# Optimization experiments

Measured on AMD Instinct MI355X. Metric: run time of the kernel, lower is better.

The kernel has to match this reference:

```python
import jax, jax.numpy as jnp
import numpy as np

DIM = 1024
DFF = 4096
B, L = 4, 4096


def _lin_init(key, din, dout):
    k1, k2 = jax.random.split(key)
    bound = 1.0 / np.sqrt(din)
    w = jax.random.uniform(k1, (din, dout), jnp.float32, -bound, bound)
    b = jax.random.uniform(k2, (dout,), jnp.float32, -bound, bound)
    return w, b


def setup_inputs() -> dict:
    key = jax.random.key(0)
    ks = jax.random.split(key, 12)
    x = jax.random.normal(ks[0], (B, L, DIM), jnp.float32)
    hidden = jax.random.normal(ks[1], (B, DIM), jnp.float32)
    w_ln_z, b_ln_z = _lin_init(ks[2], DIM, DIM)
    w_dt, b_dt = _lin_init(ks[3], DIM, DIM)
    w_y, b_y = _lin_init(ks[4], DIM, DIM)
    w_yg, b_yg = _lin_init(ks[5], DIM, DIM)
    w_ff, b_ff = _lin_init(ks[6], DIM, DFF)
    w_ffg, b_ffg = _lin_init(ks[7], DIM, DFF)
    w_ffo, b_ffo = _lin_init(ks[8], DFF, DIM)
    g_sio = jnp.ones((DIM,), jnp.float32)
    g_ffn = jnp.ones((DIM,), jnp.float32)
    return dict(x=x, hidden=hidden, w_ln_z=w_ln_z, b_ln_z=b_ln_z, w_dt=w_dt,
                b_dt=b_dt, w_y=w_y, b_y=b_y, w_yg=w_yg, b_yg=b_yg,
                w_ff=w_ff, b_ff=b_ff, w_ffg=w_ffg, b_ffg=b_ffg,
                w_ffo=w_ffo, b_ffo=b_ffo, g_sio=g_sio, g_ffn=g_ffn)


def _rmsnorm(x, g, eps=1e-6):
    return x * jax.lax.rsqrt(jnp.mean(x * x, axis=-1, keepdims=True) + eps) * g


def reference(x, hidden, w_ln_z, b_ln_z, w_dt, b_dt, w_y, b_y, w_yg, b_yg,
              w_ff, b_ff, w_ffg, b_ffg, w_ffo, b_ffo, g_sio, g_ffn):
    silu = jax.nn.silu
    sp = jax.nn.softplus
    # --- SioConv branch ---
    residual = x
    xn = _rmsnorm(x, g_sio)
    dt = xn @ w_dt + b_dt
    ln_z = -sp(-(xn @ w_ln_z + b_ln_z))
    ln_da = -sp(-dt)           # log sigmoid(dt)
    ln_o_da = -sp(dt)          # log sigmoid(-dt)
    ln_o_da_cumsum = jnp.cumsum(ln_o_da, axis=1)
    lcse = jax.lax.cumlogsumexp(ln_z + ln_da - ln_o_da_cumsum, axis=1)
    h_inner = jnp.exp(lcse + ln_o_da_cumsum)                 # [B,L,D]
    h_cross = jnp.exp(ln_o_da_cumsum) * hidden[:, None, :]   # [B,L,D]
    h = h_inner + h_cross
    y = (h @ w_y + b_y) * silu(xn @ w_yg + b_yg)
    x = y + residual
    # --- FFN branch ---
    residual = x
    xn = _rmsnorm(x, g_ffn)
    ff = ((xn @ w_ff + b_ff) * silu(xn @ w_ffg + b_ffg)) @ w_ffo + b_ffo
    x = ff + residual
    return (x, h)
```

## Files before the change

kernel.cpp:

```cpp
#include <hip/hip_runtime.h>
#include <cstdint>
#include <cstddef>

using u16 = unsigned short;
using bf16x8 = __attribute__((ext_vector_type(8))) short;
using f32x4  = __attribute__((ext_vector_type(4))) float;

__device__ __forceinline__ u16 f2bf(float f) {
  unsigned u = __float_as_uint(f);
  u += 0x7fffu + ((u >> 16) & 1u);
  return (u16)(u >> 16);
}
__device__ __forceinline__ float bf2f(u16 h) {
  return __uint_as_float(((unsigned)h) << 16);
}

__device__ __forceinline__ void gload_lds16(const void* g, void* l) {
  auto gp = reinterpret_cast<const __attribute__((address_space(1))) char*>(
      reinterpret_cast<uintptr_t>(g));
  auto lp = reinterpret_cast<__attribute__((address_space(3))) char*>(
      reinterpret_cast<uintptr_t>(l));
  __builtin_amdgcn_global_load_lds(gp, lp, 16, 0, 0);
}

__global__ __launch_bounds__(256) void transpose_to_bf16(
    const float* __restrict__ W, u16* __restrict__ WT, int din, int dout) {
  __shared__ float tile[32][33];
  const int j0 = blockIdx.x * 32;
  const int i0 = blockIdx.y * 32;
  const int tx = threadIdx.x & 31;
  const int ty = threadIdx.x >> 5;
#pragma unroll
  for (int k = 0; k < 32; k += 8)
    tile[ty + k][tx] = W[(size_t)(i0 + ty + k) * dout + (j0 + tx)];
  __syncthreads();
#pragma unroll
  for (int k = 0; k < 32; k += 8)
    WT[(size_t)(j0 + ty + k) * din + (i0 + tx)] = f2bf(tile[tx][ty + k]);
}

__global__ __launch_bounds__(256) void rmsnorm_kernel(
    const float* __restrict__ x, const float* __restrict__ g, u16* __restrict__ xn) {
  const int row = blockIdx.x;
  const float4 v = ((const float4*)(x + (size_t)row * 1024))[threadIdx.x];
  float ss = v.x * v.x + v.y * v.y + v.z * v.z + v.w * v.w;
#pragma unroll
  for (int off = 32; off > 0; off >>= 1) ss += __shfl_down(ss, off, 64);
  __shared__ float red[4];
  if ((threadIdx.x & 63) == 0) red[threadIdx.x >> 6] = ss;
  __syncthreads();
  const float rs = rsqrtf((red[0] + red[1] + red[2] + red[3]) * (1.f / 1024.f) + 1e-6f);
  const float4 gv = ((const float4*)g)[threadIdx.x];
  ushort4 o;
  o.x = f2bf(v.x * rs * gv.x);
  o.y = f2bf(v.y * rs * gv.y);
  o.z = f2bf(v.z * rs * gv.z);
  o.w = f2bf(v.w * rs * gv.w);
  ((ushort4*)(xn + (size_t)row * 1024))[threadIdx.x] = o;
}

__global__ __launch_bounds__(256) void scan_pass1(
    const u16* __restrict__ dt, const u16* __restrict__ lnz,
    float* __restrict__ P, float* __restrict__ S) {
  const int blk = blockIdx.x;
  const int dblk = blk & 3;
  const int chunk = (blk >> 2) & 63;
  const int b = blk >> 8;
  const int d = dblk * 256 + threadIdx.x;
  const size_t base = ((size_t)b * 4096 + (size_t)chunk * 64) * 1024 + d;
  float p = 1.f, s = 0.f;
#pragma unroll 8
  for (int l = 0; l < 64; ++l) {
    const float dtv = bf2f(dt[base + (size_t)l * 1024]);
    const float zv = bf2f(lnz[base + (size_t)l * 1024]);
    const float a = 1.f / (1.f + __expf(dtv));
    const float zs = 1.f / (1.f + __expf(-zv));
    const float in = (1.f - a) * zs;
    p *= a;
    s = a * s + in;
  }
  const size_t o = ((size_t)b * 64 + chunk) * 1024 + d;
  P[o] = p;
  S[o] = s;
}

__global__ __launch_bounds__(256) void scan_pass2(
    const float* __restrict__ P, const float* __restrict__ S,
    const float* __restrict__ hidden, float* __restrict__ hin) {
  const int idx = blockIdx.x * 256 + threadIdx.x;
  const int b = idx >> 10, d = idx & 1023;
  float h = hidden[idx];
#pragma unroll 8
  for (int c = 0; c < 64; ++c) {
    const size_t o = ((size_t)b * 64 + c) * 1024 + d;
    hin[o] = h;
    h = P[o] * h + S[o];
  }
}

__global__ __launch_bounds__(256) void scan_pass3(
    const u16* __restrict__ dt, const u16* __restrict__ lnz,
    const float* __restrict__ hin, float* __restrict__ h_out, u16* __restrict__ hbf) {
  const int blk = blockIdx.x;
  const int dblk = blk & 3;
  const int chunk = (blk >> 2) & 63;
  const int b = blk >> 8;
  const int d = dblk * 256 + threadIdx.x;
  const size_t base = ((size_t)b * 4096 + (size_t)chunk * 64) * 1024 + d;
  float h = hin[((size_t)b * 64 + chunk) * 1024 + d];
#pragma unroll 4
  for (int l = 0; l < 64; ++l) {
    const float dtv = bf2f(dt[base + (size_t)l * 1024]);
    const float zv = bf2f(lnz[base + (size_t)l * 1024]);
    const float a = 1.f / (1.f + __expf(dtv));
    const float zs = 1.f / (1.f + __expf(-zv));
    h = a * h + (1.f - a) * zs;
    h_out[base + (size_t)l * 1024] = h;
    hbf[base + (size_t)l * 1024] = f2bf(h);
  }
}

template <int EPI>
__global__ __launch_bounds__(512, 4) void gemm256(
    const u16* __restrict__ A, const u16* __restrict__ B,
    const float* __restrict__ bias, const u16* __restrict__ gate,
    const float* __restrict__ resid, float* __restrict__ outF,
    u16* __restrict__ outH, u16* __restrict__ outH2, u16* __restrict__ outH3,
    int ntx, int N, int K) {
  constexpr int SLOT = 16384;
  const int tid = threadIdx.x;
  const int lane = tid & 63;
  const int wid = tid >> 6;
  const int wrow = wid >> 1;
  const int wcol = wid & 1;
  const int whalf = wrow >> 1;
  const int wsub  = wrow & 1;

  const int nwg = gridDim.x;
  int id = blockIdx.x;
  id = (id & 7) * (nwg >> 3) + (id >> 3);
  const int m0 = (id / ntx) * 256;
  const int n0 = (id % ntx) * 128;

  __shared__ __align__(16) char lds[5 * SLOT];

  f32x4 acc[4][4];
#pragma unroll
  for (int m = 0; m < 4; ++m)
#pragma unroll
    for (int n = 0; n < 4; ++n) acc[m][n] = (f32x4){0.f, 0.f, 0.f, 0.f};

  bf16x8 aR[2];
  bf16x8 bR[4][2];

  int aOff[4], bOff[4];
  {
    const int lq = (lane >> 4) << 4;
#pragma unroll
    for (int m = 0; m < 4; ++m) {
      const int hr = wsub * 64 + m * 16 + (lane & 15);
      aOff[m] = hr * 128 + (lq ^ ((hr & 7) << 4));
    }
#pragma unroll
    for (int n = 0; n < 4; ++n) {
      const int hr = wcol * 64 + n * 16 + (lane & 15);
      bOff[n] = hr * 128 + (lq ^ ((hr & 7) << 4));
    }
  }

  const int row0 = tid >> 3;
  const int kb0  = ((tid & 7) * 16) ^ ((row0 & 7) << 4);
  const size_t dRow = (size_t)128 * K;
  const char* pA0 = (const char*)A + (size_t)(m0 + row0) * K * 2 + kb0;
  const char* pA1 = pA0 + (size_t)256 * K;
  const char* pB  = (const char*)B + (size_t)(n0 + row0) * K * 2 + kb0;
  const int ldst = tid * 16;

#define STAGE(PTR, SB)                                                        \
  {                                                                           \
    gload_lds16(PTR, lds + (SB) + ldst);                                      \
    gload_lds16(PTR + dRow, lds + (SB) + ldst + 8192);                        \
    PTR += 128;                                                               \
  }

#define READA(SAB, Q)                                                         \
  {                                                                           \
    const int _o = aOff[Q];                                                   \
    aR[0] = *(const bf16x8*)(lds + (SAB) + _o);                               \
    aR[1] = *(const bf16x8*)(lds + (SAB) + (_o ^ 64));                        \
  }

#define READB(SBB)                                                            \
  _Pragma("unroll") for (int n = 0; n < 4; ++n) {                             \
    const int _o = bOff[n];                                                   \
    bR[n][0] = *(const bf16x8*)(lds + (SBB) + _o);                            \
    bR[n][1] = *(const bf16x8*)(lds + (SBB) + (_o ^ 64));                     \
  }

#define MMAQ(Q)                                                               \
  __builtin_amdgcn_s_setprio(1);                                              \
  _Pragma("unroll") for (int n = 0; n < 4; ++n)                               \
  _Pragma("unroll") for (int k = 0; k < 2; ++k)                               \
      acc[Q][n] = __builtin_amdgcn_mfma_f32_16x16x32_bf16(                    \
          aR[k], bR[n][k], acc[Q][n], 0, 0, 0);                               \
  __builtin_amdgcn_s_setprio(0);

  const int NT = K >> 6;

  STAGE(pB,  0 * SLOT);
  STAGE(pA0, 1 * SLOT);
  STAGE(pA1, 2 * SLOT);
  asm volatile("s_waitcnt vmcnt(0)" ::: "memory");
  __builtin_amdgcn_s_barrier();

  int iB = 0;

  for (int t = 0; t < NT; ++t) {
    int ib1 = iB + 1 + whalf; if (ib1 >= 5) ib1 -= 5;
    const int sAb = __builtin_amdgcn_readfirstlane(ib1 * SLOT);
    const int sBb = __builtin_amdgcn_readfirstlane(iB * SLOT);
    int i0s = iB + 3; if (i0s >= 5) i0s -= 5;
    int i1s = iB + 4; if (i1s >= 5) i1s -= 5;
    const int s0 = i0s * SLOT, s1 = i1s * SLOT, s2 = iB * SLOT;
    const bool st = (t < NT - 1);
    READB(sBb);
    READA(sAb, 0);
    if (st) STAGE(pB, s0);
    MMAQ(0);
    READA(sAb, 1);
    if (st) STAGE(pA0, s1);
    MMAQ(1);
    READA(sAb, 2);
    MMAQ(2);
    __builtin_amdgcn_s_barrier();
    READA(sAb, 3);
    if (st) STAGE(pA1, s2);
    MMAQ(3);
    asm volatile("s_waitcnt vmcnt(0)" ::: "memory");
    __builtin_amdgcn_s_barrier();
    iB += 3; if (iB >= 5) iB -= 5;
  }

#pragma unroll
  for (int m = 0; m < 4; ++m) {
#pragma unroll
    for (int n = 0; n < 4; ++n) {
      const int col = n0 + wcol * 64 + n * 16 + (lane & 15);
#pragma unroll
      for (int j = 0; j < 4; ++j) {
        const int row = m0 + wrow * 64 + m * 16 + ((lane >> 4) << 2) + j;
        const float v = acc[m][n][j] + bias[col];
        if constexpr (EPI == 5) {
          const int rg = col >> 10;
          const size_t o = (size_t)row * 1024 + (col & 1023);
          if (rg == 0) outH[o] = f2bf(v);
          else if (rg == 1) outH2[o] = f2bf(v);
          else outH3[o] = f2bf(v);
        } else {
          const size_t o = (size_t)row * N + col;
          if constexpr (EPI == 2) {
            const float gt = bf2f(gate[o]);
            outF[o] = v * (gt / (1.f + __expf(-gt))) + resid[o];
          } else if constexpr (EPI == 6) {
            outH[o] = f2bf(v / (1.f + __expf(-v)));
          } else if constexpr (EPI == 7) {
            outH[o] = f2bf(v * bf2f(gate[o]));
          } else if constexpr (EPI == 4) {
            outF[o] = v + outF[o];
          }
        }
      }
    }
  }
#undef STAGE
#undef READA
#undef READB
#undef MMAQ
}

extern "C" void kernel_launch(void* const* d_in, const int* in_sizes, int n_in,
                              void* d_out, int out_size, void* d_ws, size_t ws_size,
                              hipStream_t stream) {
  const float* x      = (const float*)d_in[0];
  const float* hidden = (const float*)d_in[1];
  const float* w_ln_z = (const float*)d_in[2];
  const float* b_ln_z = (const float*)d_in[3];
  const float* w_dt   = (const float*)d_in[4];
  const float* b_dt   = (const float*)d_in[5];
  const float* w_y    = (const float*)d_in[6];
  const float* b_y    = (const float*)d_in[7];
  const float* w_yg   = (const float*)d_in[8];
  const float* b_yg   = (const float*)d_in[9];
  const float* w_ff   = (const float*)d_in[10];
  const float* b_ff   = (const float*)d_in[11];
  const float* w_ffg  = (const float*)d_in[12];
  const float* b_ffg  = (const float*)d_in[13];
  const float* w_ffo  = (const float*)d_in[14];
  const float* b_ffo  = (const float*)d_in[15];
  const float* g_sio  = (const float*)d_in[16];
  const float* g_ffn  = (const float*)d_in[17];

  char* ws = (char*)d_ws;
  const size_t MB = 1ull << 20;
  u16*   WT_cat = (u16*)(ws + 0 * MB);
  u16*   WT_y   = (u16*)(ws + 8 * MB);
  u16*   WT_ff  = (u16*)(ws + 10 * MB);
  u16*   WT_ffg = (u16*)(ws + 18 * MB);
  u16*   WT_ffo = (u16*)(ws + 26 * MB);
  float* b_cat  = (float*)(ws + 34 * MB);
  u16*   xn     = (u16*)(ws + 36 * MB);
  u16*   dt16   = (u16*)(ws + 68 * MB);
  u16*   lnzb   = (u16*)(ws + 100 * MB);
  u16*   ygb    = (u16*)(ws + 132 * MB);
  u16*   hbf    = (u16*)(ws + 164 * MB);
  float* Pc     = (float*)(ws + 196 * MB);
  float* Sc     = (float*)(ws + 197 * MB);
  float* hin    = (float*)(ws + 198 * MB);
  u16*   gs     = (u16*)(ws + 68 * MB);

  float* x_out = (float*)d_out;
  float* h_out = (float*)d_out + (size_t)4 * 4096 * 1024;

  const int M = 16384, D = 1024, F = 4096;
  const dim3 tb(256);

  transpose_to_bf16<<<dim3(32, 32), tb, 0, stream>>>(w_dt, WT_cat, D, D);
  transpose_to_bf16<<<dim3(32, 32), tb, 0, stream>>>(w_ln_z, WT_cat + 1024 * 1024, D, D);
  transpose_to_bf16<<<dim3(32, 32), tb, 0, stream>>>(w_yg, WT_cat + 2 * 1024 * 1024, D, D);
  transpose_to_bf16<<<dim3(32, 32), tb, 0, stream>>>(w_y, WT_y, D, D);
  transpose_to_bf16<<<dim3(128, 32), tb, 0, stream>>>(w_ff, WT_ff, D, F);
  transpose_to_bf16<<<dim3(128, 32), tb, 0, stream>>>(w_ffg, WT_ffg, D, F);
  transpose_to_bf16<<<dim3(32, 128), tb, 0, stream>>>(w_ffo, WT_ffo, F, D);
  (void)hipMemcpyAsync(b_cat, b_dt, D * 4, hipMemcpyDeviceToDevice, stream);
  (void)hipMemcpyAsync(b_cat + 1024, b_ln_z, D * 4, hipMemcpyDeviceToDevice, stream);
  (void)hipMemcpyAsync(b_cat + 2048, b_yg, D * 4, hipMemcpyDeviceToDevice, stream);

  rmsnorm_kernel<<<M, tb, 0, stream>>>(x, g_sio, xn);

  gemm256<5><<<dim3(64 * 24), 512, 0, stream>>>(xn, WT_cat, b_cat, nullptr, nullptr,
                                                nullptr, dt16, lnzb, ygb, 24, 3072, D);

  scan_pass1<<<1024, tb, 0, stream>>>(dt16, lnzb, Pc, Sc);
  scan_pass2<<<16, tb, 0, stream>>>(Pc, Sc, hidden, hin);
  scan_pass3<<<1024, tb, 0, stream>>>(dt16, lnzb, hin, h_out, hbf);

  gemm256<2><<<dim3(64 * 8), 512, 0, stream>>>(hbf, WT_y, b_y, ygb, x,
                                               x_out, nullptr, nullptr, nullptr, 8, D, D);

  rmsnorm_kernel<<<M, tb, 0, stream>>>(x_out, g_ffn, xn);

  gemm256<6><<<dim3(64 * 32), 512, 0, stream>>>(xn, WT_ffg, b_ffg, nullptr, nullptr,
                                                nullptr, gs, nullptr, nullptr, 32, F, D);
  gemm256<7><<<dim3(64 * 32), 512, 0, stream>>>(xn, WT_ff, b_ff, gs, nullptr,
                                                nullptr, gs, nullptr, nullptr, 32, F, D);
  gemm256<4><<<dim3(64 * 8), 512, 0, stream>>>(gs, WT_ffo, b_ffo, nullptr, nullptr,
                                               x_out, nullptr, nullptr, nullptr, 8, D, F);
}
```

Baseline: 745.9 us.

## Load GEMM B fragments directly from global into registers, bypassing LDS

The B operand tiles are no longer staged through shared memory. Each wave now reads its B fragments straight from global memory into registers, in two halves per K tile. Only the two A sub-tiles go through the 5-slot LDS ring, which now advances by two slots per iteration. This removes B's LDS traffic and one barrier. In exchange, A fragments are re-read from LDS twice per tile, and the mfma chain now waits on global-load latency, which shares the vmcnt counter with the async A staging loads.

```diff
diff --git a/kernel.cpp b/kernel.cpp
--- a/kernel.cpp
+++ b/kernel.cpp
@@ -151,29 +151,27 @@
     for (int n = 0; n < 4; ++n) acc[m][n] = (f32x4){0.f, 0.f, 0.f, 0.f};
 
   bf16x8 aR[2];
-  bf16x8 bR[4][2];
-
-  int aOff[4], bOff[4];
+  bf16x8 bR[2][2];
+
+  int aOff0;
   {
     const int lq = (lane >> 4) << 4;
-#pragma unroll
-    for (int m = 0; m < 4; ++m) {
-      const int hr = wsub * 64 + m * 16 + (lane & 15);
-      aOff[m] = hr * 128 + (lq ^ ((hr & 7) << 4));
-    }
-#pragma unroll
-    for (int n = 0; n < 4; ++n) {
-      const int hr = wcol * 64 + n * 16 + (lane & 15);
-      bOff[n] = hr * 128 + (lq ^ ((hr & 7) << 4));
-    }
-  }
+    const int hr = wsub * 64 + (lane & 15);
+    aOff0 = hr * 128 + (lq ^ ((hr & 7) << 4));
+  }
+
+  const char* pBf[4];
+#pragma unroll
+  for (int j = 0; j < 4; ++j)
+    pBf[j] = (const char*)B +
+             (size_t)(n0 + wcol * 64 + j * 16 + (lane & 15)) * K * 2 +
+             ((lane >> 4) << 4);
 
   const int row0 = tid >> 3;
   const int kb0  = ((tid & 7) * 16) ^ ((row0 & 7) << 4);
   const size_t dRow = (size_t)128 * K;
   const char* pA0 = (const char*)A + (size_t)(m0 + row0) * K * 2 + kb0;
   const char* pA1 = pA0 + (size_t)256 * K;
-  const char* pB  = (const char*)B + (size_t)(n0 + row0) * K * 2 + kb0;
   const int ldst = tid * 16;
 
 #define STAGE(PTR, SB)                                                        \
@@ -185,60 +183,60 @@
 
 #define READA(SAB, Q)                                                         \
   {                                                                           \
-    const int _o = aOff[Q];                                                   \
+    const int _o = aOff0 + (Q) * 2048;                                        \
     aR[0] = *(const bf16x8*)(lds + (SAB) + _o);                               \
     aR[1] = *(const bf16x8*)(lds + (SAB) + (_o ^ 64));                        \
   }
 
-#define READB(SBB)                                                            \
-  _Pragma("unroll") for (int n = 0; n < 4; ++n) {                             \
-    const int _o = bOff[n];                                                   \
-    bR[n][0] = *(const bf16x8*)(lds + (SBB) + _o);                            \
-    bR[n][1] = *(const bf16x8*)(lds + (SBB) + (_o ^ 64));                     \
-  }
-
-#define MMAQ(Q)                                                               \
+#define READBG(H)                                                             \
+  _Pragma("unroll") for (int n = 0; n < 2; ++n) {                             \
+    const char* _p = pBf[(H) * 2 + n];                                        \
+    bR[n][0] = *(const bf16x8*)_p;                                            \
+    bR[n][1] = *(const bf16x8*)(_p + 64);                                     \
+  }
+
+#define MMAH(Q, H)                                                            \
   __builtin_amdgcn_s_setprio(1);                                              \
-  _Pragma("unroll") for (int n = 0; n < 4; ++n)                               \
+  _Pragma("unroll") for (int n = 0; n < 2; ++n)                               \
   _Pragma("unroll") for (int k = 0; k < 2; ++k)                               \
-      acc[Q][n] = __builtin_amdgcn_mfma_f32_16x16x32_bf16(                    \
-          aR[k], bR[n][k], acc[Q][n], 0, 0, 0);                               \
+      acc[Q][(H) * 2 + n] = __builtin_amdgcn_mfma_f32_16x16x32_bf16(          \
+          aR[k], bR[n][k], acc[Q][(H) * 2 + n], 0, 0, 0);                     \
   __builtin_amdgcn_s_setprio(0);
 
   const int NT = K >> 6;
 
-  STAGE(pB,  0 * SLOT);
-  STAGE(pA0, 1 * SLOT);
-  STAGE(pA1, 2 * SLOT);
+  STAGE(pA0, 0 * SLOT);
+  STAGE(pA1, 1 * SLOT);
   asm volatile("s_waitcnt vmcnt(0)" ::: "memory");
   __builtin_amdgcn_s_barrier();
 
-  int iB = 0;
+  int iA0 = 0;
 
   for (int t = 0; t < NT; ++t) {
-    int ib1 = iB + 1 + whalf; if (ib1 >= 5) ib1 -= 5;
-    const int sAb = __builtin_amdgcn_readfirstlane(ib1 * SLOT);
-    const int sBb = __builtin_amdgcn_readfirstlane(iB * SLOT);
-    int i0s = iB + 3; if (i0s >= 5) i0s -= 5;
-    int i1s = iB + 4; if (i1s >= 5) i1s -= 5;
-    const int s0 = i0s * SLOT, s1 = i1s * SLOT, s2 = iB * SLOT;
+    int ra = iA0 + whalf; if (ra >= 5) ra -= 5;
+    const int sAb = __builtin_amdgcn_readfirstlane(ra * SLOT);
+    int s2 = iA0 + 2; if (s2 >= 5) s2 -= 5;
+    int s3 = iA0 + 3; if (s3 >= 5) s3 -= 5;
     const bool st = (t < NT - 1);
-    READB(sBb);
-    READA(sAb, 0);
-    if (st) STAGE(pB, s0);
-    MMAQ(0);
-    READA(sAb, 1);
-    if (st) STAGE(pA0, s1);
-    MMAQ(1);
-    READA(sAb, 2);
-    MMAQ(2);
-    __builtin_amdgcn_s_barrier();
-    READA(sAb, 3);
-    if (st) STAGE(pA1, s2);
-    MMAQ(3);
+    READBG(0);
+    if (st) {
+      STAGE(pA0, s2 * SLOT);
+      STAGE(pA1, s3 * SLOT);
+    }
+    READA(sAb, 0); MMAH(0, 0);
+    READA(sAb, 1); MMAH(1, 0);
+    READA(sAb, 2); MMAH(2, 0);
+    READA(sAb, 3); MMAH(3, 0);
+    READBG(1);
+    READA(sAb, 0); MMAH(0, 1);
+    READA(sAb, 1); MMAH(1, 1);
+    READA(sAb, 2); MMAH(2, 1);
+    READA(sAb, 3); MMAH(3, 1);
+#pragma unroll
+    for (int j = 0; j < 4; ++j) pBf[j] += 128;
     asm volatile("s_waitcnt vmcnt(0)" ::: "memory");
     __builtin_amdgcn_s_barrier();
-    iB += 3; if (iB >= 5) iB -= 5;
+    iA0 += 2; if (iA0 >= 5) iA0 -= 5;
   }
 
 #pragma unroll
@@ -274,8 +272,8 @@
   }
 #undef STAGE
 #undef READA
-#undef READB
-#undef MMAQ
+#undef READBG
+#undef MMAH
 }
 
 extern "C" void kernel_launch(void* const* d_in, const int* in_sizes, int n_in,
```

Result: slower. 1.331 ms (+78.4%).

## Replace 256x128 GEMM tile with 128x128 tile using 256 threads

Applied to the files above, without the earlier changes.

Shrinks the GEMM work-group tile from 256x128 with 8 waves to 128x128 with 4 waves. The LDS ring drops from five slots to three, and the staging schedule is reorganized so A and B tiles rotate through them. Grids double in block count. The smaller tile is meant to reduce LDS use and improve occupancy and load balance, but it lowers data reuse per block and raises global and LDS traffic per FLOP.

```diff
diff --git a/kernel.cpp b/kernel.cpp
--- a/kernel.cpp
+++ b/kernel.cpp
@@ -121,7 +121,7 @@
 }
 
 template <int EPI>
-__global__ __launch_bounds__(512, 4) void gemm256(
+__global__ __launch_bounds__(256, 3) void gemm128(
     const u16* __restrict__ A, const u16* __restrict__ B,
     const float* __restrict__ bias, const u16* __restrict__ gate,
     const float* __restrict__ resid, float* __restrict__ outF,
@@ -133,16 +133,14 @@
   const int wid = tid >> 6;
   const int wrow = wid >> 1;
   const int wcol = wid & 1;
-  const int whalf = wrow >> 1;
-  const int wsub  = wrow & 1;
 
   const int nwg = gridDim.x;
   int id = blockIdx.x;
   id = (id & 7) * (nwg >> 3) + (id >> 3);
-  const int m0 = (id / ntx) * 256;
+  const int m0 = (id / ntx) * 128;
   const int n0 = (id % ntx) * 128;
 
-  __shared__ __align__(16) char lds[5 * SLOT];
+  __shared__ __align__(16) char lds[3 * SLOT];
 
   f32x4 acc[4][4];
 #pragma unroll
@@ -153,46 +151,41 @@
   bf16x8 aR[2];
   bf16x8 bR[4][2];
 
-  int aOff[4], bOff[4];
+  int aOff0, bOff0;
   {
     const int lq = (lane >> 4) << 4;
-#pragma unroll
-    for (int m = 0; m < 4; ++m) {
-      const int hr = wsub * 64 + m * 16 + (lane & 15);
-      aOff[m] = hr * 128 + (lq ^ ((hr & 7) << 4));
-    }
-#pragma unroll
-    for (int n = 0; n < 4; ++n) {
-      const int hr = wcol * 64 + n * 16 + (lane & 15);
-      bOff[n] = hr * 128 + (lq ^ ((hr & 7) << 4));
-    }
+    const int ha = wrow * 64 + (lane & 15);
+    aOff0 = ha * 128 + (lq ^ ((ha & 7) << 4));
+    const int hb = wcol * 64 + (lane & 15);
+    bOff0 = hb * 128 + (lq ^ ((hb & 7) << 4));
   }
 
   const int row0 = tid >> 3;
   const int kb0  = ((tid & 7) * 16) ^ ((row0 & 7) << 4);
-  const size_t dRow = (size_t)128 * K;
-  const char* pA0 = (const char*)A + (size_t)(m0 + row0) * K * 2 + kb0;
-  const char* pA1 = pA0 + (size_t)256 * K;
-  const char* pB  = (const char*)B + (size_t)(n0 + row0) * K * 2 + kb0;
+  const size_t d32 = (size_t)64 * K;
+  const char* pA = (const char*)A + (size_t)(m0 + row0) * K * 2 + kb0;
+  const char* pB = (const char*)B + (size_t)(n0 + row0) * K * 2 + kb0;
   const int ldst = tid * 16;
 
 #define STAGE(PTR, SB)                                                        \
   {                                                                           \
     gload_lds16(PTR, lds + (SB) + ldst);                                      \
-    gload_lds16(PTR + dRow, lds + (SB) + ldst + 8192);                        \
+    gload_lds16(PTR + d32, lds + (SB) + ldst + 4096);                         \
+    gload_lds16(PTR + 2 * d32, lds + (SB) + ldst + 8192);                     \
+    gload_lds16(PTR + 3 * d32, lds + (SB) + ldst + 12288);                    \
     PTR += 128;                                                               \
   }
 
 #define READA(SAB, Q)                                                         \
   {                                                                           \
-    const int _o = aOff[Q];                                                   \
+    const int _o = aOff0 + (Q) * 2048;                                        \
     aR[0] = *(const bf16x8*)(lds + (SAB) + _o);                               \
     aR[1] = *(const bf16x8*)(lds + (SAB) + (_o ^ 64));                        \
   }
 
 #define READB(SBB)                                                            \
   _Pragma("unroll") for (int n = 0; n < 4; ++n) {                             \
-    const int _o = bOff[n];                                                   \
+    const int _o = bOff0 + n * 2048;                                          \
     bR[n][0] = *(const bf16x8*)(lds + (SBB) + _o);                            \
     bR[n][1] = *(const bf16x8*)(lds + (SBB) + (_o ^ 64));                     \
   }
@@ -207,38 +200,31 @@
 
   const int NT = K >> 6;
 
-  STAGE(pB,  0 * SLOT);
-  STAGE(pA0, 1 * SLOT);
-  STAGE(pA1, 2 * SLOT);
+  STAGE(pA, 0 * SLOT);
+  STAGE(pB, 1 * SLOT);
   asm volatile("s_waitcnt vmcnt(0)" ::: "memory");
   __builtin_amdgcn_s_barrier();
 
-  int iB = 0;
+  int sA = 0;
 
   for (int t = 0; t < NT; ++t) {
-    int ib1 = iB + 1 + whalf; if (ib1 >= 5) ib1 -= 5;
-    const int sAb = __builtin_amdgcn_readfirstlane(ib1 * SLOT);
-    const int sBb = __builtin_amdgcn_readfirstlane(iB * SLOT);
-    int i0s = iB + 3; if (i0s >= 5) i0s -= 5;
-    int i1s = iB + 4; if (i1s >= 5) i1s -= 5;
-    const int s0 = i0s * SLOT, s1 = i1s * SLOT, s2 = iB * SLOT;
+    int sB = sA + 1; if (sB >= 3) sB -= 3;
+    int sN = sA + 2; if (sN >= 3) sN -= 3;
+    const int sAb = __builtin_amdgcn_readfirstlane(sA * SLOT);
+    const int sBb = __builtin_amdgcn_readfirstlane(sB * SLOT);
     const bool st = (t < NT - 1);
     READB(sBb);
     READA(sAb, 0);
-    if (st) STAGE(pB, s0);
+    if (st) STAGE(pA, sN * SLOT);
     MMAQ(0);
-    READA(sAb, 1);
-    if (st) STAGE(pA0, s1);
-    MMAQ(1);
-    READA(sAb, 2);
-    MMAQ(2);
+    READA(sAb, 1); MMAQ(1);
+    READA(sAb, 2); MMAQ(2);
+    READA(sAb, 3); MMAQ(3);
     __builtin_amdgcn_s_barrier();
-    READA(sAb, 3);
-    if (st) STAGE(pA1, s2);
-    MMAQ(3);
+    if (st) STAGE(pB, sA * SLOT);
     asm volatile("s_waitcnt vmcnt(0)" ::: "memory");
     __builtin_amdgcn_s_barrier();
-    iB += 3; if (iB >= 5) iB -= 5;
+    sA += 2; if (sA >= 3) sA -= 3;
   }
 
 #pragma unroll
@@ -337,22 +323,22 @@
 
   rmsnorm_kernel<<<M, tb, 0, stream>>>(x, g_sio, xn);
 
-  gemm256<5><<<dim3(64 * 24), 512, 0, stream>>>(xn, WT_cat, b_cat, nullptr, nullptr,
+  gemm128<5><<<dim3(128 * 24), tb, 0, stream>>>(xn, WT_cat, b_cat, nullptr, nullptr,
                                                 nullptr, dt16, lnzb, ygb, 24, 3072, D);
 
   scan_pass1<<<1024, tb, 0, stream>>>(dt16, lnzb, Pc, Sc);
   scan_pass2<<<16, tb, 0, stream>>>(Pc, Sc, hidden, hin);
   scan_pass3<<<1024, tb, 0, stream>>>(dt16, lnzb, hin, h_out, hbf);
 
-  gemm256<2><<<dim3(64 * 8), 512, 0, stream>>>(hbf, WT_y, b_y, ygb, x,
+  gemm128<2><<<dim3(128 * 8), tb, 0, stream>>>(hbf, WT_y, b_y, ygb, x,
                                                x_out, nullptr, nullptr, nullptr, 8, D, D);
 
   rmsnorm_kernel<<<M, tb, 0, stream>>>(x_out, g_ffn, xn);
 
-  gemm256<6><<<dim3(64 * 32), 512, 0, stream>>>(xn, WT_ffg, b_ffg, nullptr, nullptr,
+  gemm128<6><<<dim3(128 * 32), tb, 0, stream>>>(xn, WT_ffg, b_ffg, nullptr, nullptr,
                                                 nullptr, gs, nullptr, nullptr, 32, F, D);
-  gemm256<7><<<dim3(64 * 32), 512, 0, stream>>>(xn, WT_ff, b_ff, gs, nullptr,
+  gemm128<7><<<dim3(128 * 32), tb, 0, stream>>>(xn, WT_ff, b_ff, gs, nullptr,
                                                 nullptr, gs, nullptr, nullptr, 32, F, D);
-  gemm256<4><<<dim3(64 * 8), 512, 0, stream>>>(gs, WT_ffo, b_ffo, nullptr, nullptr,
+  gemm128<4><<<dim3(128 * 8), tb, 0, stream>>>(gs, WT_ffo, b_ffo, nullptr, nullptr,
                                                x_out, nullptr, nullptr, nullptr, 8, D, F);
 }
```

Result: slower. 847.3 us (+13.6%).

## Fuse FFN up and gate GEMMs into one dual-B kernel with SwiGLU epilogue

Applied to the files above, without the earlier changes.

Replaces the two back-to-back FFN GEMMs (gate with SiLU written to bf16, then up projection multiplied by the reread gate) with one kernel. It loads a shared A tile and two 64-wide B tiles per stage, keeps two accumulator sets, and applies bias, SiLU and the product in the epilogue. This drops the second read of the normalized activations and the write then reread of the intermediate gate tensor. The price is narrower N tiles with twice the grid and more accumulator registers per thread. LDS offset arrays are also replaced by a base offset plus constant stride to save registers.

```diff
diff --git a/kernel.cpp b/kernel.cpp
--- a/kernel.cpp
+++ b/kernel.cpp
@@ -153,19 +153,13 @@
   bf16x8 aR[2];
   bf16x8 bR[4][2];
 
-  int aOff[4], bOff[4];
+  int aOff0, bOff0;
   {
     const int lq = (lane >> 4) << 4;
-#pragma unroll
-    for (int m = 0; m < 4; ++m) {
-      const int hr = wsub * 64 + m * 16 + (lane & 15);
-      aOff[m] = hr * 128 + (lq ^ ((hr & 7) << 4));
-    }
-#pragma unroll
-    for (int n = 0; n < 4; ++n) {
-      const int hr = wcol * 64 + n * 16 + (lane & 15);
-      bOff[n] = hr * 128 + (lq ^ ((hr & 7) << 4));
-    }
+    const int ha = wsub * 64 + (lane & 15);
+    aOff0 = ha * 128 + (lq ^ ((ha & 7) << 4));
+    const int hb = wcol * 64 + (lane & 15);
+    bOff0 = hb * 128 + (lq ^ ((hb & 7) << 4));
   }
 
   const int row0 = tid >> 3;
@@ -185,14 +179,14 @@
 
 #define READA(SAB, Q)                                                         \
   {                                                                           \
-    const int _o = aOff[Q];                                                   \
+    const int _o = aOff0 + (Q) * 2048;                                        \
     aR[0] = *(const bf16x8*)(lds + (SAB) + _o);                               \
     aR[1] = *(const bf16x8*)(lds + (SAB) + (_o ^ 64));                        \
   }
 
 #define READB(SBB)                                                            \
   _Pragma("unroll") for (int n = 0; n < 4; ++n) {                             \
-    const int _o = bOff[n];                                                   \
+    const int _o = bOff0 + n * 2048;                                          \
     bR[n][0] = *(const bf16x8*)(lds + (SBB) + _o);                            \
     bR[n][1] = *(const bf16x8*)(lds + (SBB) + (_o ^ 64));                     \
   }
@@ -261,10 +255,6 @@
           if constexpr (EPI == 2) {
             const float gt = bf2f(gate[o]);
             outF[o] = v * (gt / (1.f + __expf(-gt))) + resid[o];
-          } else if constexpr (EPI == 6) {
-            outH[o] = f2bf(v / (1.f + __expf(-v)));
-          } else if constexpr (EPI == 7) {
-            outH[o] = f2bf(v * bf2f(gate[o]));
           } else if constexpr (EPI == 4) {
             outF[o] = v + outF[o];
           }
@@ -276,6 +266,157 @@
 #undef READA
 #undef READB
 #undef MMAQ
+}
+
+__global__ __launch_bounds__(512, 4) void gemm_dual(
+    const u16* __restrict__ A, const u16* __restrict__ B1, const u16* __restrict__ B2,
+    const float* __restrict__ bias1, const float* __restrict__ bias2,
+    u16* __restrict__ outH, int ntx, int N, int K) {
+  constexpr int SLOT = 16384;
+  const int tid = threadIdx.x;
+  const int lane = tid & 63;
+  const int wid = tid >> 6;
+  const int wrow = wid >> 1;
+  const int wcol = wid & 1;
+  const int whalf = wrow >> 1;
+  const int wsub  = wrow & 1;
+
+  const int nwg = gridDim.x;
+  int id = blockIdx.x;
+  id = (id & 7) * (nwg >> 3) + (id >> 3);
+  const int m0 = (id / ntx) * 256;
+  const int n0 = (id % ntx) * 64;
+
+  __shared__ __align__(16) char lds[5 * SLOT];
+
+  f32x4 acc1[4][2], acc2[4][2];
+#pragma unroll
+  for (int m = 0; m < 4; ++m)
+#pragma unroll
+    for (int n = 0; n < 2; ++n) {
+      acc1[m][n] = (f32x4){0.f, 0.f, 0.f, 0.f};
+      acc2[m][n] = (f32x4){0.f, 0.f, 0.f, 0.f};
+    }
+
+  bf16x8 aR[2];
+  bf16x8 b1R[2][2], b2R[2][2];
+
+  int aOff0, bOff0;
+  {
+    const int lq = (lane >> 4) << 4;
+    const int ha = wsub * 64 + (lane & 15);
+    aOff0 = ha * 128 + (lq ^ ((ha & 7) << 4));
+    const int hb = wcol * 32 + (lane & 15);
+    bOff0 = hb * 128 + (lq ^ ((hb & 7) << 4));
+  }
+
+  const int row0 = tid >> 3;
+  const int kb0  = ((tid & 7) * 16) ^ ((row0 & 7) << 4);
+  const size_t dRow = (size_t)128 * K;
+  const char* pA0 = (const char*)A + (size_t)(m0 + row0) * K * 2 + kb0;
+  const char* pA1 = pA0 + (size_t)256 * K;
+  const char* pB1 = (const char*)B1 + (size_t)(n0 + row0) * K * 2 + kb0;
+  const char* pB2 = (const char*)B2 + (size_t)(n0 + row0) * K * 2 + kb0;
+  const int ldst = tid * 16;
+
+#define STAGEA(PTR, SB)                                                       \
+  {                                                                           \
+    gload_lds16(PTR, lds + (SB) + ldst);                                      \
+    gload_lds16(PTR + dRow, lds + (SB) + ldst + 8192);                        \
+    PTR += 128;                                                               \
+  }
+#define STAGEB(PTR, SB, OFF)                                                  \
+  {                                                                           \
+    gload_lds16(PTR, lds + (SB) + (OFF) + ldst);                              \
+    PTR += 128;                                                               \
+  }
+
+#define READA(SAB, Q)                                                         \
+  {                                                                           \
+    const int _o = aOff0 + (Q) * 2048;                                        \
+    aR[0] = *(const bf16x8*)(lds + (SAB) + _o);                               \
+    aR[1] = *(const bf16x8*)(lds + (SAB) + (_o ^ 64));                        \
+  }
+
+#define READBD(SBB)                                                           \
+  _Pragma("unroll") for (int n = 0; n < 2; ++n) {                             \
+    const int _o = bOff0 + n * 2048;                                          \
+    b1R[n][0] = *(const bf16x8*)(lds + (SBB) + _o);                           \
+    b1R[n][1] = *(const bf16x8*)(lds + (SBB) + (_o ^ 64));                    \
+    b2R[n][0] = *(const bf16x8*)(lds + (SBB) + 8192 + _o);                    \
+    b2R[n][1] = *(const bf16x8*)(lds + (SBB) + 8192 + (_o ^ 64));             \
+  }
+
+#define MMAD(Q)                                                               \
+  __builtin_amdgcn_s_setprio(1);                                              \
+  _Pragma("unroll") for (int n = 0; n < 2; ++n)                               \
+  _Pragma("unroll") for (int k = 0; k < 2; ++k) {                             \
+    acc1[Q][n] = __builtin_amdgcn_mfma_f32_16x16x32_bf16(                     \
+        aR[k], b1R[n][k], acc1[Q][n], 0, 0, 0);                               \
+    acc2[Q][n] = __builtin_amdgcn_mfma_f32_16x16x32_bf16(                     \
+        aR[k], b2R[n][k], acc2[Q][n], 0, 0, 0);                               \
+  }                                                                           \
+  __builtin_amdgcn_s_setprio(0);
+
+  const int NT = K >> 6;
+
+  STAGEB(pB1, 0 * SLOT, 0);
+  STAGEB(pB2, 0 * SLOT, 8192);
+  STAGEA(pA0, 1 * SLOT);
+  STAGEA(pA1, 2 * SLOT);
+  asm volatile("s_waitcnt vmcnt(0)" ::: "memory");
+  __builtin_amdgcn_s_barrier();
+
+  int iB = 0;
+
+  for (int t = 0; t < NT; ++t) {
+    int ib1 = iB + 1 + whalf; if (ib1 >= 5) ib1 -= 5;
+    const int sAb = __builtin_amdgcn_readfirstlane(ib1 * SLOT);
+    const int sBb = __builtin_amdgcn_readfirstlane(iB * SLOT);
+    int i0s = iB + 3; if (i0s >= 5) i0s -= 5;
+    int i1s = iB + 4; if (i1s >= 5) i1s -= 5;
+    const int s0 = i0s * SLOT, s1 = i1s * SLOT, s2 = iB * SLOT;
+    const bool st = (t < NT - 1);
+    READBD(sBb);
+    READA(sAb, 0);
+    if (st) {
+      STAGEB(pB1, s0, 0);
+      STAGEB(pB2, s0, 8192);
+    }
+    MMAD(0);
+    READA(sAb, 1);
+    if (st) STAGEA(pA0, s1);
+    MMAD(1);
+    READA(sAb, 2);
+    MMAD(2);
+    __builtin_amdgcn_s_barrier();
+    READA(sAb, 3);
+    if (st) STAGEA(pA1, s2);
+    MMAD(3);
+    asm volatile("s_waitcnt vmcnt(0)" ::: "memory");
+    __builtin_amdgcn_s_barrier();
+    iB += 3; if (iB >= 5) iB -= 5;
+  }
+
+#pragma unroll
+  for (int m = 0; m < 4; ++m) {
+#pragma unroll
+    for (int n = 0; n < 2; ++n) {
+      const int col = n0 + wcol * 32 + n * 16 + (lane & 15);
+#pragma unroll
+      for (int j = 0; j < 4; ++j) {
+        const int row = m0 + wrow * 64 + m * 16 + ((lane >> 4) << 2) + j;
+        const float v1 = acc1[m][n][j] + bias1[col];
+        const float v2 = acc2[m][n][j] + bias2[col];
+        outH[(size_t)row * N + col] = f2bf(v1 * (v2 / (1.f + __expf(-v2))));
+      }
+    }
+  }
+#undef STAGEA
+#undef STAGEB
+#undef READA
+#undef READBD
+#undef MMAD
 }
 
 extern "C" void kernel_launch(void* const* d_in, const int* in_sizes, int n_in,
@@ -349,10 +490,9 @@
 
   rmsnorm_kernel<<<M, tb, 0, stream>>>(x_out, g_ffn, xn);
 
-  gemm256<6><<<dim3(64 * 32), 512, 0, stream>>>(xn, WT_ffg, b_ffg, nullptr, nullptr,
-                                                nullptr, gs, nullptr, nullptr, 32, F, D);
-  gemm256<7><<<dim3(64 * 32), 512, 0, stream>>>(xn, WT_ff, b_ff, gs, nullptr,
-                                                nullptr, gs, nullptr, nullptr, 32, F, D);
+  gemm_dual<<<dim3(64 * 64), 512, 0, stream>>>(xn, WT_ff, WT_ffg, b_ff, b_ffg,
+                                               gs, 64, F, D);
+
   gemm256<4><<<dim3(64 * 8), 512, 0, stream>>>(gs, WT_ffo, b_ffo, nullptr, nullptr,
                                                x_out, nullptr, nullptr, nullptr, 8, D, F);
 }
```

Result: faster. 719.4 us (-3.6%).
